# Kernel tuning notes

Hardware: AMD Instinct MI355X
Metric: run time of the kernel (lower is better)

The kernel has to match this reference:

```python
import jax, jax.numpy as jnp
import numpy as np

C = 128
NUM_GROUPS = 32
EPS = 1e-6


def setup_inputs() -> dict:
    key = jax.random.key(0)
    ks = jax.random.split(key, 6)
    B, H, W = 8, 64, 64
    x = jax.random.normal(ks[0], (B, C, H, W), dtype=jnp.float32)
    # 1x1 conv weights stored as [out_c, in_c] (kernel spatial dims are 1)
    fan_avg = C  # fan_in == fan_out == C for 1x1 conv
    bound = np.sqrt(3.0 / fan_avg)
    wq = jax.random.uniform(ks[1], (C, C), jnp.float32, -bound, bound)
    wk = jax.random.uniform(ks[2], (C, C), jnp.float32, -bound, bound)
    wv = jax.random.uniform(ks[3], (C, C), jnp.float32, -bound, bound)
    # proj_out has init_scale=0.0 -> near-zero init; use tiny random instead to test math
    wo = jax.random.uniform(ks[4], (C, C), jnp.float32, -bound, bound) * 1e-3
    bq = jnp.zeros((C,), jnp.float32)
    bk = jnp.zeros((C,), jnp.float32)
    bv = jnp.zeros((C,), jnp.float32)
    bo = jnp.zeros((C,), jnp.float32)
    gamma = jnp.ones((C,), jnp.float32)
    beta = jnp.zeros((C,), jnp.float32)
    return {"x": x, "gamma": gamma, "beta": beta,
            "wq": wq, "bq": bq, "wk": wk, "bk": bk,
            "wv": wv, "bv": bv, "wo": wo, "bo": bo}


def _group_norm(x, gamma, beta):
    B, Ch, H, W = x.shape
    g = NUM_GROUPS
    xg = x.reshape(B, g, Ch // g, H, W)
    mean = jnp.mean(xg, axis=(2, 3, 4), keepdims=True)
    var = jnp.var(xg, axis=(2, 3, 4), keepdims=True)
    xn = ((xg - mean) * jax.lax.rsqrt(var + EPS)).reshape(B, Ch, H, W)
    return xn * gamma[None, :, None, None] + beta[None, :, None, None]


def _conv1x1(x, w, b):
    # x: [B,C,H,W], w: [O,C], b: [O]
    return jnp.einsum('bchw,oc->bohw', x, w) + b[None, :, None, None]


def reference(x, gamma, beta, wq, bq, wk, bk, wv, bv, wo, bo):
    B, Ch, H, W = x.shape
    n = H * W
    h = _group_norm(x, gamma, beta)
    q = _conv1x1(h, wq, bq).reshape(B, Ch, n)
    k = _conv1x1(h, wk, bk).reshape(B, Ch, n)
    v = _conv1x1(h, wv, bv).reshape(B, Ch, n)
    # attn[b, i, j] = sum_c q[b,c,i] * k[b,c,j] / sqrt(C)
    attn = jnp.einsum('bci,bcj->bij', q, k) * (float(Ch) ** -0.5)
    attn = jax.nn.softmax(attn, axis=-1)
    # h[b,c,i] = sum_j v[b,c,j] * attn[b,i,j]
    out = jnp.einsum('bcj,bij->bci', v, attn).reshape(B, Ch, H, W)
    out = _conv1x1(out, wo, bo)
    return x + out
```

## Files before the change

kernel.cpp:

```cpp
#include <hip/hip_runtime.h>


typedef float f32x4 __attribute__((ext_vector_type(4)));
typedef short short8 __attribute__((ext_vector_type(8)));
typedef _Float16 half8 __attribute__((ext_vector_type(8)));
typedef _Float16 half2t __attribute__((ext_vector_type(2)));
typedef unsigned short ush;
typedef unsigned short ush4 __attribute__((ext_vector_type(4)));
typedef unsigned int uint4t __attribute__((ext_vector_type(4)));
typedef int int8v __attribute__((ext_vector_type(8)));

union V8U {
  uint4t h[2];
  int8v v;
};

__device__ __forceinline__ ush f2bf(float f) {
  unsigned u = __builtin_bit_cast(unsigned, f);
  u = (u + 0x7FFFu + ((u >> 16) & 1u)) >> 16;
  return (ush)u;
}
__device__ __forceinline__ float bf2f(ush v) {
  unsigned u = ((unsigned)v) << 16;
  return __builtin_bit_cast(float, u);
}
__device__ __forceinline__ unsigned f2fp8(float x) {
  unsigned u = __builtin_bit_cast(unsigned, x);
  unsigned s = (u >> 24) & 0x80u;
  unsigned au = u & 0x7fffffffu;
  if (au < 0x3A800000u) return s;
  if (au >= 0x43E00000u) return s | 0x7Eu;
  int e = (int)(au >> 23) - 127;
  if (e < -6) {
    float a = __builtin_bit_cast(float, au);
    int m = (int)(a * 512.0f + 0.5f);
    if (m >= 8) return s | 0x08u;
    return s | (unsigned)m;
  }
  unsigned keep = au >> 20, rem = au & 0xFFFFFu;
  keep += (rem > 0x80000u) || ((rem == 0x80000u) && (keep & 1u));
  int ef = (int)(keep >> 3) - 127;
  if (ef >= 8 && ((ef > 8) || ((keep & 7u) == 7u))) return s | 0x7Eu;
  return s | (unsigned)(((ef + 7) << 3) | (int)(keep & 7u));
}
__device__ __forceinline__ void async16(const void* g, void* l) {
  __builtin_amdgcn_global_load_lds(
      (const __attribute__((address_space(1))) unsigned int*)g,
      (__attribute__((address_space(3))) unsigned int*)l, 16, 0, 0);
}

__global__ __launch_bounds__(256) void gn_stats_kernel(
    const float* __restrict__ x, const float* __restrict__ gamma,
    const float* __restrict__ beta, const float* __restrict__ wo,
    const float* __restrict__ wq, const float* __restrict__ wk,
    const float* __restrict__ wv, float* __restrict__ scale_c,
    float* __restrict__ shift_c, ush* __restrict__ wobh,
    ush* __restrict__ wqb, ush* __restrict__ wkb, ush* __restrict__ wvb) {
  int bg = blockIdx.x;
  int b = bg >> 5, g = bg & 31;
  int tid = threadIdx.x;
  if (bg < 64) {
    int m = bg >> 4;
    int v4 = ((bg & 15) * 256 + tid) * 4;
    const float* src = m == 0 ? wo : (m == 1 ? wq : (m == 2 ? wk : wv));
    float4 w4 = *(const float4*)(src + v4);
    ush4 pk;
    if (m == 0) {
      pk.x = __builtin_bit_cast(ush, (_Float16)w4.x);
      pk.y = __builtin_bit_cast(ush, (_Float16)w4.y);
      pk.z = __builtin_bit_cast(ush, (_Float16)w4.z);
      pk.w = __builtin_bit_cast(ush, (_Float16)w4.w);
      *(ush4*)(wobh + v4) = pk;
    } else {
      pk.x = f2bf(w4.x); pk.y = f2bf(w4.y);
      pk.z = f2bf(w4.z); pk.w = f2bf(w4.w);
      ush* dst = m == 1 ? wqb : (m == 2 ? wkb : wvb);
      *(ush4*)(dst + v4) = pk;
    }
  }
  const float4* base = (const float4*)(x + (size_t)bg * 16384);
  float s = 0.f, sq = 0.f;
#pragma unroll
  for (int p = 0; p < 16; ++p) {
    float4 v = base[p * 256 + tid];
    s += (v.x + v.y) + (v.z + v.w);
    sq += (v.x * v.x + v.y * v.y) + (v.z * v.z + v.w * v.w);
  }
#pragma unroll
  for (int off = 32; off > 0; off >>= 1) {
    s += __shfl_down(s, off);
    sq += __shfl_down(sq, off);
  }
  __shared__ float rs[4], rq[4], mv[2];
  int w = tid >> 6, lane = tid & 63;
  if (lane == 0) { rs[w] = s; rq[w] = sq; }
  __syncthreads();
  if (tid == 0) {
    float S = (rs[0] + rs[1]) + (rs[2] + rs[3]);
    float Q = (rq[0] + rq[1]) + (rq[2] + rq[3]);
    float mean = S * (1.f / 16384.f);
    float var = Q * (1.f / 16384.f) - mean * mean;
    mv[0] = mean;
    mv[1] = rsqrtf(var + 1e-6f);
  }
  __syncthreads();
  if (tid < 4) {
    int c = (g << 2) + tid;
    float sc = mv[1] * gamma[c];
    scale_c[(b << 7) + c] = sc;
    shift_c[(b << 7) + c] = beta[c] - mv[0] * sc;
  }
}

__global__ __launch_bounds__(256) void qkv_kernel(
    const float* __restrict__ x, const float* __restrict__ scale_c,
    const float* __restrict__ shift_c, const ush* __restrict__ wqb,
    const ush* __restrict__ wkb, const ush* __restrict__ wvb,
    const float* __restrict__ bq, const float* __restrict__ bk,
    const float* __restrict__ bv, char* __restrict__ Qt8,
    char* __restrict__ Kt8, _Float16* __restrict__ Vh) {
  __shared__ __align__(16) ush hs[64 * 136];
  __shared__ __align__(16) ush wol[128 * 136];
  char* hs8 = (char*)hs;
  int bx = blockIdx.x;
  int type = bx >> 9;
  int rb = bx & 511;
  int b = rb >> 6, i0 = (rb & 63) << 6;
  int tid = threadIdx.x;
  int w = tid >> 6, lane = tid & 63, ln15 = lane & 15, quad = lane >> 4;

#pragma unroll
  for (int p = 0; p < 8; ++p) {
    int id = p * 256 + tid;
    int i = id & 63;
    int g8 = id >> 6;
    int c0 = g8 << 2;
    const float* xp = x + (((size_t)((b << 7) + c0)) << 12) + i0 + i;
    ush4 pk4;
#pragma unroll
    for (int e = 0; e < 4; ++e) {
      float h = xp[(size_t)e << 12] * scale_c[(b << 7) + c0 + e] +
                shift_c[(b << 7) + c0 + e];
      pk4[e] = f2bf(h);
    }
    int pg = g8 ^ ((i & 15) << 1);
    *(ush4*)(hs8 + i * 272 + pg * 8) = pk4;
  }
  const ush* Wb = type == 0 ? wqb : (type == 1 ? wkb : wvb);
#pragma unroll
  for (int p = 0; p < 8; ++p) {
    int cid = p * 256 + tid;
    int o = cid >> 4, ch = (cid & 15) << 3;
    *(uint4t*)&wol[o * 136 + ch] = *(const uint4t*)(Wb + (o << 7) + ch);
  }
  __syncthreads();

#define HS_FRAG(row, dc) \
  (*(const short8*)(hs8 + (row) * 272 + (((((dc)*4 + quad)) ^ ((row)&15)) << 4)))

  if (type < 2) {
    f32x4 acc[8] = {};
    int hrow = w * 16 + ln15;
#pragma unroll
    for (int dc = 0; dc < 4; ++dc) {
      short8 af = HS_FRAG(hrow, dc);
#pragma unroll
      for (int nb = 0; nb < 8; ++nb) {
        short8 bf = *(const short8*)&wol[(nb * 16 + ln15) * 136 + dc * 32 + quad * 8];
        acc[nb] = __builtin_amdgcn_mfma_f32_16x16x32_bf16(af, bf, acc[nb], 0, 0, 0);
      }
    }
    const float* bias = type == 0 ? bq : bk;
    char* dst8 = type == 0 ? Qt8 : Kt8;
    __syncthreads();
#pragma unroll
    for (int nb = 0; nb < 8; ++nb) {
      int o = nb * 16 + ln15;
      float bi = bias[o];
#pragma unroll
      for (int r = 0; r < 4; ++r) {
        float val = acc[nb][r] + bi;
        if (type == 0) val *= 0.12751742f;
        hs8[(w * 16 + quad * 4 + r) * 144 + o] = (char)f2fp8(val);
      }
    }
    __syncthreads();
    int i = tid >> 2, seg = tid & 3;
    uint4 d0 = *(const uint4*)(hs8 + i * 144 + seg * 32);
    uint4 d1 = *(const uint4*)(hs8 + i * 144 + seg * 32 + 16);
    char* drow = dst8 + (((size_t)((b << 12) + i0 + i)) << 7) + seg * 32;
    *(uint4*)drow = d0;
    *(uint4*)(drow + 16) = d1;
  } else {
    f32x4 acc[8] = {};
    int hrow = w * 16 + ln15;
#pragma unroll
    for (int dc = 0; dc < 4; ++dc) {
      short8 bf = HS_FRAG(hrow, dc);
#pragma unroll
      for (int mb = 0; mb < 8; ++mb) {
        short8 af = *(const short8*)&wol[(mb * 16 + ln15) * 136 + dc * 32 + quad * 8];
        acc[mb] = __builtin_amdgcn_mfma_f32_16x16x32_bf16(af, bf, acc[mb], 0, 0, 0);
      }
    }
#pragma unroll
    for (int mb = 0; mb < 8; ++mb) {
#pragma unroll
      for (int r = 0; r < 4; ++r) {
        int o = mb * 16 + quad * 4 + r;
        float val = acc[mb][r] + bv[o];
        Vh[(((size_t)((b << 7) + o)) << 12) + i0 + w * 16 + ln15] = (_Float16)val;
      }
    }
  }
#undef HS_FRAG
}

__global__ __launch_bounds__(256, 2) void attn_kernel(
    const char* __restrict__ Qt8, const char* __restrict__ Kt8,
    const _Float16* __restrict__ Vh, ush* __restrict__ po,
    float* __restrict__ lw) {
  __shared__ __align__(16) char ksb[2][4096];
  __shared__ __align__(16) _Float16 vsb[2][4096];
  int bx = blockIdx.x;
  int b = bx & 7, qt = (bx >> 3) & 15, ksid = bx >> 7;
  int tid = threadIdx.x;
  int w = tid >> 6, lane = tid & 63, ln15 = lane & 15, quad = lane >> 4;
  int qbase = (qt << 8) + (w << 6);
  int j0 = ksid << 10;

  int8v qf[4];
#pragma unroll
  for (int ih = 0; ih < 4; ++ih) {
    const char* qrow =
        Qt8 + (((size_t)((b << 12) + qbase + ih * 16 + ln15)) << 7) + quad * 32;
    V8U u;
    u.h[0] = *(const uint4t*)(qrow);
    u.h[1] = *(const uint4t*)(qrow + 16);
    qf[ih] = u.v;
  }

  int kj = (w << 3) + (lane >> 3);
  int kh = (kj & 3) | (((kj >> 3) & 1) << 2);
  int kg = (lane & 7) ^ kh;
  const char* ksrc = Kt8 + (((size_t)((b << 12) + j0 + kj)) << 7) + (kg << 4);
  int d0r = (w << 5) + (lane >> 2);
  int d1r = d0r + 16;
  int vg0 = (lane & 3) ^ (((d0r >> 1) + (d0r >> 3)) & 3);
  int vg1 = (lane & 3) ^ (((d1r >> 1) + (d1r >> 3)) & 3);
  const _Float16* vsrc0 =
      Vh + (((size_t)((b << 7) + d0r)) << 12) + j0 + (vg0 << 3);
  const _Float16* vsrc1 =
      Vh + (((size_t)((b << 7) + d1r)) << 12) + j0 + (vg1 << 3);
  char* kdA = &ksb[0][0] + (w << 10);
  char* kdB = &ksb[1][0] + (w << 10);
  char* vdA0 = (char*)&vsb[0][0] + ((w * 2 + 0) << 10);
  char* vdA1 = (char*)&vsb[0][0] + ((w * 2 + 1) << 10);
  char* vdB0 = (char*)&vsb[1][0] + ((w * 2 + 0) << 10);
  char* vdB1 = (char*)&vsb[1][0] + ((w * 2 + 1) << 10);

  async16(ksrc, kdA);
  async16(vsrc0, vdA0);
  async16(vsrc1, vdA1);
  __syncthreads();

  f32x4 O[4][8] = {};
  float lsum[4] = {0.f, 0.f, 0.f, 0.f};
  const f32x4 SINIT = {-7.2134752f, -7.2134752f, -7.2134752f, -7.2134752f};
  int r0 = ((ln15 >> 2) << 3) + (ln15 & 3), r1 = r0 + 4;
  int hr = (ln15 & 3) | (((ln15 >> 2) & 1) << 2);
  int g0 = ((2 * quad) ^ hr) << 4;
  int g1 = ((2 * quad + 1) ^ hr) << 4;

  for (int jt = 0; jt < 32; ++jt) {
    int buf = jt & 1;
    if (jt + 1 < 32) {
      ksrc += 4096;
      vsrc0 += 32;
      vsrc1 += 32;
      if (buf == 0) {
        async16(ksrc, kdB);
        async16(vsrc0, vdB0);
        async16(vsrc1, vdB1);
      } else {
        async16(ksrc, kdA);
        async16(vsrc0, vdA0);
        async16(vsrc1, vdA1);
      }
    }
    const char* kb = &ksb[buf][0];
    const char* vb = (const char*)&vsb[buf][0];

    V8U ka, kc;
    ka.h[0] = *(const uint4t*)(kb + r0 * 128 + g0);
    ka.h[1] = *(const uint4t*)(kb + r0 * 128 + g1);
    kc.h[0] = *(const uint4t*)(kb + r1 * 128 + g0);
    kc.h[1] = *(const uint4t*)(kb + r1 * 128 + g1);
    f32x4 S[4][2];
#pragma unroll
    for (int ih = 0; ih < 4; ++ih) {
      S[ih][0] = __builtin_amdgcn_mfma_scale_f32_16x16x128_f8f6f4(
          ka.v, qf[ih], SINIT, 0, 0, 0, 0x7F7F7F7F, 0, 0x7F7F7F7F);
      S[ih][1] = __builtin_amdgcn_mfma_scale_f32_16x16x128_f8f6f4(
          kc.v, qf[ih], SINIT, 0, 0, 0, 0x7F7F7F7F, 0, 0x7F7F7F7F);
    }

    half8 pf[4];
#pragma unroll
    for (int ih = 0; ih < 4; ++ih) {
      float p0 = __builtin_amdgcn_exp2f(S[ih][0][0]);
      float p1 = __builtin_amdgcn_exp2f(S[ih][0][1]);
      float p2 = __builtin_amdgcn_exp2f(S[ih][0][2]);
      float p3 = __builtin_amdgcn_exp2f(S[ih][0][3]);
      float p4 = __builtin_amdgcn_exp2f(S[ih][1][0]);
      float p5 = __builtin_amdgcn_exp2f(S[ih][1][1]);
      float p6 = __builtin_amdgcn_exp2f(S[ih][1][2]);
      float p7 = __builtin_amdgcn_exp2f(S[ih][1][3]);
      lsum[ih] += ((p0 + p1) + (p2 + p3)) + ((p4 + p5) + (p6 + p7));
      uint4t pw;
      pw.x = __builtin_bit_cast(unsigned, __builtin_amdgcn_cvt_pkrtz(p0, p1));
      pw.y = __builtin_bit_cast(unsigned, __builtin_amdgcn_cvt_pkrtz(p2, p3));
      pw.z = __builtin_bit_cast(unsigned, __builtin_amdgcn_cvt_pkrtz(p4, p5));
      pw.w = __builtin_bit_cast(unsigned, __builtin_amdgcn_cvt_pkrtz(p6, p7));
      pf[ih] = __builtin_bit_cast(half8, pw);
    }
#pragma unroll
    for (int nb = 0; nb < 8; ++nb) {
      int d = nb * 16 + ln15;
      int sd = ((d >> 1) + (d >> 3)) & 3;
      half8 vf = *(const half8*)(vb + d * 64 + ((quad ^ sd) << 4));
#pragma unroll
      for (int ih = 0; ih < 4; ++ih)
        O[ih][nb] = __builtin_amdgcn_mfma_f32_16x16x32_f16(vf, pf[ih], O[ih][nb], 0, 0, 0);
    }
    __syncthreads();
  }

#pragma unroll
  for (int ih = 0; ih < 4; ++ih) {
    float l = lsum[ih];
    l += __shfl_xor(l, 16);
    l += __shfl_xor(l, 32);
    if (quad == 0) lw[(ksid << 15) + (b << 12) + qbase + ih * 16 + ln15] = l;
    int i = qbase + ih * 16 + ln15;
    size_t rowb = (((size_t)((ksid * 8 + b)) << 12) + i) << 7;
#pragma unroll
    for (int nb = 0; nb < 8; ++nb) {
      ush4 pk;
      pk.x = __builtin_bit_cast(ush, (_Float16)O[ih][nb][0]);
      pk.y = __builtin_bit_cast(ush, (_Float16)O[ih][nb][1]);
      pk.z = __builtin_bit_cast(ush, (_Float16)O[ih][nb][2]);
      pk.w = __builtin_bit_cast(ush, (_Float16)O[ih][nb][3]);
      *(ush4*)(po + rowb + nb * 16 + quad * 4) = pk;
    }
  }
}

__global__ __launch_bounds__(256) void proj_kernel(
    const float* __restrict__ x, const ush* __restrict__ po,
    const float* __restrict__ lw, const ush* __restrict__ wobh,
    const float* __restrict__ bo, float* __restrict__ out) {
  int bx = blockIdx.x;
  int oh = bx & 1;
  int bi = bx >> 1;
  int b = bi >> 6, i0 = (bi & 63) << 6;
  int tid = threadIdx.x;
  int w = tid >> 6, lane = tid & 63, ln15 = lane & 15, quad = lane >> 4;
  int i = i0 + w * 16 + ln15;
  float rl = 0.f;
#pragma unroll
  for (int s = 0; s < 4; ++s) rl += lw[(s << 15) + (b << 12) + i];
  _Float16 rh = (_Float16)(1.f / rl);

  f32x4 acc[4] = {};
#pragma unroll
  for (int dc = 0; dc < 4; ++dc) {
    size_t base = ((size_t)i << 7) + dc * 32 + quad * 8;
    half8 vs = *(const half8*)(po + (((size_t)b) << 19) + base);
#pragma unroll
    for (int s = 1; s < 4; ++s)
      vs = vs + *(const half8*)(po + (((size_t)(s * 8 + b)) << 19) + base);
    half8 bfv = vs * rh;
#pragma unroll
    for (int mb = 0; mb < 4; ++mb) {
      half8 af = *(const half8*)&wobh[(((oh * 4 + mb) * 16 + ln15) << 7) +
                                      dc * 32 + quad * 8];
      acc[mb] = __builtin_amdgcn_mfma_f32_16x16x32_f16(af, bfv, acc[mb], 0, 0, 0);
    }
  }
#pragma unroll
  for (int mb = 0; mb < 4; ++mb) {
#pragma unroll
    for (int r = 0; r < 4; ++r) {
      int o = (oh * 4 + mb) * 16 + quad * 4 + r;
      size_t idx = (((size_t)(b << 7) + o) << 12) + i;
      out[idx] = x[idx] + acc[mb][r] + bo[o];
    }
  }
}

extern "C" void kernel_launch(void* const* d_in, const int* in_sizes, int n_in,
                              void* d_out, int out_size, void* d_ws,
                              size_t ws_size, hipStream_t stream) {
  const float* x = (const float*)d_in[0];
  const float* gamma = (const float*)d_in[1];
  const float* beta = (const float*)d_in[2];
  const float* wq = (const float*)d_in[3];
  const float* bq = (const float*)d_in[4];
  const float* wk = (const float*)d_in[5];
  const float* bk = (const float*)d_in[6];
  const float* wv = (const float*)d_in[7];
  const float* bv = (const float*)d_in[8];
  const float* wo = (const float*)d_in[9];
  const float* bo = (const float*)d_in[10];
  float* out = (float*)d_out;

  const size_t NE = (size_t)8 * 4096 * 128;
  char* Qt8 = (char*)d_ws;
  char* Kt8 = Qt8 + NE;
  _Float16* Vh = (_Float16*)(Kt8 + NE);
  ush* po = (ush*)(Vh + NE);
  float* lwp = (float*)(po + 4 * NE);
  float* scale_c = lwp + 4 * 32768;
  float* shift_c = scale_c + 1024;
  ush* wobh = (ush*)(shift_c + 1024);
  ush* wqb = wobh + 16384;
  ush* wkb = wqb + 16384;
  ush* wvb = wkb + 16384;

  gn_stats_kernel<<<256, 256, 0, stream>>>(x, gamma, beta, wo, wq, wk, wv,
                                           scale_c, shift_c, wobh, wqb, wkb,
                                           wvb);
  qkv_kernel<<<1536, 256, 0, stream>>>(x, scale_c, shift_c, wqb, wkb, wvb, bq,
                                       bk, bv, Qt8, Kt8, Vh);
  attn_kernel<<<512, 256, 0, stream>>>(Qt8, Kt8, Vh, po, lwp);
  proj_kernel<<<1024, 256, 0, stream>>>(x, po, lwp, wobh, bo, out);
}
```

Baseline: 186.4 us.

## Use FP8 for V and probabilities in attention PV matmul with larger key tiles

V is now stored as FP8 instead of FP16, and the softmax probabilities are packed to FP8. The P·V product uses the 16x16x128 scaled FP8 MFMA, which needs a per-wave LDS round-trip to reshape P into the operand layout. Key/value tiles grow from 32 to 128 keys per iteration, giving 8 iterations instead of 32 and fewer barriers. Costs are lower accuracy for P and V, and extra LDS traffic and footprint, about 72KB per block, which may limit occupancy.

```diff
diff --git a/kernel.cpp b/kernel.cpp
--- a/kernel.cpp
+++ b/kernel.cpp
@@ -4,7 +4,6 @@
 typedef float f32x4 __attribute__((ext_vector_type(4)));
 typedef short short8 __attribute__((ext_vector_type(8)));
 typedef _Float16 half8 __attribute__((ext_vector_type(8)));
-typedef _Float16 half2t __attribute__((ext_vector_type(2)));
 typedef unsigned short ush;
 typedef unsigned short ush4 __attribute__((ext_vector_type(4)));
 typedef unsigned int uint4t __attribute__((ext_vector_type(4)));
@@ -14,15 +13,15 @@
   uint4t h[2];
   int8v v;
 };
+union P8U {
+  unsigned long long l[4];
+  int8v v;
+};
 
 __device__ __forceinline__ ush f2bf(float f) {
   unsigned u = __builtin_bit_cast(unsigned, f);
   u = (u + 0x7FFFu + ((u >> 16) & 1u)) >> 16;
   return (ush)u;
-}
-__device__ __forceinline__ float bf2f(ush v) {
-  unsigned u = ((unsigned)v) << 16;
-  return __builtin_bit_cast(float, u);
 }
 __device__ __forceinline__ unsigned f2fp8(float x) {
   unsigned u = __builtin_bit_cast(unsigned, x);
@@ -118,7 +117,7 @@
     const ush* __restrict__ wkb, const ush* __restrict__ wvb,
     const float* __restrict__ bq, const float* __restrict__ bk,
     const float* __restrict__ bv, char* __restrict__ Qt8,
-    char* __restrict__ Kt8, _Float16* __restrict__ Vh) {
+    char* __restrict__ Kt8, char* __restrict__ Vh8) {
   __shared__ __align__(16) ush hs[64 * 136];
   __shared__ __align__(16) ush wol[128 * 136];
   char* hs8 = (char*)hs;
@@ -209,7 +208,8 @@
       for (int r = 0; r < 4; ++r) {
         int o = mb * 16 + quad * 4 + r;
         float val = acc[mb][r] + bv[o];
-        Vh[(((size_t)((b << 7) + o)) << 12) + i0 + w * 16 + ln15] = (_Float16)val;
+        Vh8[(((size_t)((b << 7) + o)) << 12) + i0 + w * 16 + ln15] =
+            (char)f2fp8(val);
       }
     }
   }
@@ -218,10 +218,9 @@
 
 __global__ __launch_bounds__(256, 2) void attn_kernel(
     const char* __restrict__ Qt8, const char* __restrict__ Kt8,
-    const _Float16* __restrict__ Vh, ush* __restrict__ po,
+    const char* __restrict__ Vh8, ush* __restrict__ po,
     float* __restrict__ lw) {
-  __shared__ __align__(16) char ksb[2][4096];
-  __shared__ __align__(16) _Float16 vsb[2][4096];
+  __shared__ __align__(16) char smem[73728];
   int bx = blockIdx.x;
   int b = bx & 7, qt = (bx >> 3) & 15, ksid = bx >> 7;
   int tid = threadIdx.x;
@@ -244,24 +243,23 @@
   int kh = (kj & 3) | (((kj >> 3) & 1) << 2);
   int kg = (lane & 7) ^ kh;
   const char* ksrc = Kt8 + (((size_t)((b << 12) + j0 + kj)) << 7) + (kg << 4);
-  int d0r = (w << 5) + (lane >> 2);
-  int d1r = d0r + 16;
-  int vg0 = (lane & 3) ^ (((d0r >> 1) + (d0r >> 3)) & 3);
-  int vg1 = (lane & 3) ^ (((d1r >> 1) + (d1r >> 3)) & 3);
-  const _Float16* vsrc0 =
-      Vh + (((size_t)((b << 7) + d0r)) << 12) + j0 + (vg0 << 3);
-  const _Float16* vsrc1 =
-      Vh + (((size_t)((b << 7) + d1r)) << 12) + j0 + (vg1 << 3);
-  char* kdA = &ksb[0][0] + (w << 10);
-  char* kdB = &ksb[1][0] + (w << 10);
-  char* vdA0 = (char*)&vsb[0][0] + ((w * 2 + 0) << 10);
-  char* vdA1 = (char*)&vsb[0][0] + ((w * 2 + 1) << 10);
-  char* vdB0 = (char*)&vsb[1][0] + ((w * 2 + 0) << 10);
-  char* vdB1 = (char*)&vsb[1][0] + ((w * 2 + 1) << 10);
-
-  async16(ksrc, kdA);
-  async16(vsrc0, vdA0);
-  async16(vsrc1, vdA1);
+  int vrow = (w << 3) + (lane >> 3);
+  int hv_dma = ((lane >> 3) & 3) | ((w & 1) << 2);
+  int vgd = (lane & 7) ^ hv_dma;
+  const char* vsrc =
+      Vh8 + (((size_t)((b << 7) + vrow)) << 12) + j0 + (vgd << 4);
+
+  char* Kb0 = smem;
+  char* Kb1 = smem + 16384;
+  char* Vb0 = smem + 32768;
+  char* Vb1 = smem + 49152;
+  char* Pw = smem + 65536 + (w << 11);
+
+#pragma unroll
+  for (int c = 0; c < 4; ++c) {
+    async16(ksrc + c * 4096, Kb0 + c * 4096 + (w << 10));
+    async16(vsrc + (size_t)c * 131072, Vb0 + c * 4096 + (w << 10));
+  }
   __syncthreads();
 
   f32x4 O[4][8] = {};
@@ -271,67 +269,84 @@
   int hr = (ln15 & 3) | (((ln15 >> 2) & 1) << 2);
   int g0 = ((2 * quad) ^ hr) << 4;
   int g1 = ((2 * quad + 1) ^ hr) << 4;
-
-  for (int jt = 0; jt < 32; ++jt) {
+  int hv_r = (ln15 & 3) | (((ln15 >> 3) & 1) << 2);
+  int vg0 = ((2 * quad) ^ hv_r) << 4;
+  int vg1 = ((2 * quad + 1) ^ hv_r) << 4;
+
+  unsigned pf8a[4][4][2];
+
+  for (int jt = 0; jt < 8; ++jt) {
     int buf = jt & 1;
-    if (jt + 1 < 32) {
-      ksrc += 4096;
-      vsrc0 += 32;
-      vsrc1 += 32;
-      if (buf == 0) {
-        async16(ksrc, kdB);
-        async16(vsrc0, vdB0);
-        async16(vsrc1, vdB1);
-      } else {
-        async16(ksrc, kdA);
-        async16(vsrc0, vdA0);
-        async16(vsrc1, vdA1);
-      }
-    }
-    const char* kb = &ksb[buf][0];
-    const char* vb = (const char*)&vsb[buf][0];
-
-    V8U ka, kc;
-    ka.h[0] = *(const uint4t*)(kb + r0 * 128 + g0);
-    ka.h[1] = *(const uint4t*)(kb + r0 * 128 + g1);
-    kc.h[0] = *(const uint4t*)(kb + r1 * 128 + g0);
-    kc.h[1] = *(const uint4t*)(kb + r1 * 128 + g1);
-    f32x4 S[4][2];
+    char* Kbc = buf ? Kb1 : Kb0;
+    char* Vbc = buf ? Vb1 : Vb0;
+    if (jt < 7) {
+      ksrc += 16384;
+      vsrc += 128;
+      char* Kbn = buf ? Kb0 : Kb1;
+      char* Vbn = buf ? Vb0 : Vb1;
+#pragma unroll
+      for (int c = 0; c < 4; ++c) {
+        async16(ksrc + c * 4096, Kbn + c * 4096 + (w << 10));
+        async16(vsrc + (size_t)c * 131072, Vbn + c * 4096 + (w << 10));
+      }
+    }
+
+#pragma unroll
+    for (int s = 0; s < 4; ++s) {
+      const char* kb = Kbc + s * 4096;
+      V8U ka, kc;
+      ka.h[0] = *(const uint4t*)(kb + r0 * 128 + g0);
+      ka.h[1] = *(const uint4t*)(kb + r0 * 128 + g1);
+      kc.h[0] = *(const uint4t*)(kb + r1 * 128 + g0);
+      kc.h[1] = *(const uint4t*)(kb + r1 * 128 + g1);
+#pragma unroll
+      for (int ih = 0; ih < 4; ++ih) {
+        f32x4 S0 = __builtin_amdgcn_mfma_scale_f32_16x16x128_f8f6f4(
+            ka.v, qf[ih], SINIT, 0, 0, 0, 0x7F7F7F7F, 0, 0x7F7F7F7F);
+        f32x4 S1 = __builtin_amdgcn_mfma_scale_f32_16x16x128_f8f6f4(
+            kc.v, qf[ih], SINIT, 0, 0, 0, 0x7F7F7F7F, 0, 0x7F7F7F7F);
+        float p0 = __builtin_amdgcn_exp2f(S0[0]);
+        float p1 = __builtin_amdgcn_exp2f(S0[1]);
+        float p2 = __builtin_amdgcn_exp2f(S0[2]);
+        float p3 = __builtin_amdgcn_exp2f(S0[3]);
+        float p4 = __builtin_amdgcn_exp2f(S1[0]);
+        float p5 = __builtin_amdgcn_exp2f(S1[1]);
+        float p6 = __builtin_amdgcn_exp2f(S1[2]);
+        float p7 = __builtin_amdgcn_exp2f(S1[3]);
+        lsum[ih] += ((p0 + p1) + (p2 + p3)) + ((p4 + p5) + (p6 + p7));
+        unsigned lo = (unsigned)__builtin_amdgcn_cvt_pk_fp8_f32(p0, p1, 0, false);
+        lo = (unsigned)__builtin_amdgcn_cvt_pk_fp8_f32(p2, p3, (int)lo, true);
+        unsigned hi = (unsigned)__builtin_amdgcn_cvt_pk_fp8_f32(p4, p5, 0, false);
+        hi = (unsigned)__builtin_amdgcn_cvt_pk_fp8_f32(p6, p7, (int)hi, true);
+        pf8a[ih][s][0] = lo;
+        pf8a[ih][s][1] = hi;
+      }
+    }
+
 #pragma unroll
     for (int ih = 0; ih < 4; ++ih) {
-      S[ih][0] = __builtin_amdgcn_mfma_scale_f32_16x16x128_f8f6f4(
-          ka.v, qf[ih], SINIT, 0, 0, 0, 0x7F7F7F7F, 0, 0x7F7F7F7F);
-      S[ih][1] = __builtin_amdgcn_mfma_scale_f32_16x16x128_f8f6f4(
-          kc.v, qf[ih], SINIT, 0, 0, 0, 0x7F7F7F7F, 0, 0x7F7F7F7F);
-    }
-
-    half8 pf[4];
-#pragma unroll
-    for (int ih = 0; ih < 4; ++ih) {
-      float p0 = __builtin_amdgcn_exp2f(S[ih][0][0]);
-      float p1 = __builtin_amdgcn_exp2f(S[ih][0][1]);
-      float p2 = __builtin_amdgcn_exp2f(S[ih][0][2]);
-      float p3 = __builtin_amdgcn_exp2f(S[ih][0][3]);
-      float p4 = __builtin_amdgcn_exp2f(S[ih][1][0]);
-      float p5 = __builtin_amdgcn_exp2f(S[ih][1][1]);
-      float p6 = __builtin_amdgcn_exp2f(S[ih][1][2]);
-      float p7 = __builtin_amdgcn_exp2f(S[ih][1][3]);
-      lsum[ih] += ((p0 + p1) + (p2 + p3)) + ((p4 + p5) + (p6 + p7));
-      uint4t pw;
-      pw.x = __builtin_bit_cast(unsigned, __builtin_amdgcn_cvt_pkrtz(p0, p1));
-      pw.y = __builtin_bit_cast(unsigned, __builtin_amdgcn_cvt_pkrtz(p2, p3));
-      pw.z = __builtin_bit_cast(unsigned, __builtin_amdgcn_cvt_pkrtz(p4, p5));
-      pw.w = __builtin_bit_cast(unsigned, __builtin_amdgcn_cvt_pkrtz(p6, p7));
-      pf[ih] = __builtin_bit_cast(half8, pw);
-    }
-#pragma unroll
-    for (int nb = 0; nb < 8; ++nb) {
-      int d = nb * 16 + ln15;
-      int sd = ((d >> 1) + (d >> 3)) & 3;
-      half8 vf = *(const half8*)(vb + d * 64 + ((quad ^ sd) << 4));
-#pragma unroll
-      for (int ih = 0; ih < 4; ++ih)
-        O[ih][nb] = __builtin_amdgcn_mfma_f32_16x16x32_f16(vf, pf[ih], O[ih][nb], 0, 0, 0);
+#pragma unroll
+      for (int s = 0; s < 4; ++s) {
+        unsigned long long pr =
+            ((unsigned long long)pf8a[ih][s][1] << 32) | pf8a[ih][s][0];
+        *(unsigned long long*)(Pw + ln15 * 128 +
+                               ((((s << 2) + quad) ^ ln15) << 3)) = pr;
+      }
+      P8U pu;
+#pragma unroll
+      for (int c = 0; c < 4; ++c)
+        pu.l[c] = *(const unsigned long long*)(
+            Pw + ln15 * 128 + ((((quad << 2) + c) ^ ln15) << 3));
+      int8v pfv = pu.v;
+#pragma unroll
+      for (int nb = 0; nb < 8; ++nb) {
+        int d = nb * 16 + ln15;
+        V8U va;
+        va.h[0] = *(const uint4t*)(Vbc + d * 128 + vg0);
+        va.h[1] = *(const uint4t*)(Vbc + d * 128 + vg1);
+        O[ih][nb] = __builtin_amdgcn_mfma_scale_f32_16x16x128_f8f6f4(
+            va.v, pfv, O[ih][nb], 0, 0, 0, 0x7F7F7F7F, 0, 0x7F7F7F7F);
+      }
     }
     __syncthreads();
   }
@@ -418,8 +433,8 @@
   const size_t NE = (size_t)8 * 4096 * 128;
   char* Qt8 = (char*)d_ws;
   char* Kt8 = Qt8 + NE;
-  _Float16* Vh = (_Float16*)(Kt8 + NE);
-  ush* po = (ush*)(Vh + NE);
+  char* Vh8 = Kt8 + NE;
+  ush* po = (ush*)(Vh8 + NE);
   float* lwp = (float*)(po + 4 * NE);
   float* scale_c = lwp + 4 * 32768;
   float* shift_c = scale_c + 1024;
@@ -432,7 +447,7 @@
                                            scale_c, shift_c, wobh, wqb, wkb,
                                            wvb);
   qkv_kernel<<<1536, 256, 0, stream>>>(x, scale_c, shift_c, wqb, wkb, wvb, bq,
-                                       bk, bv, Qt8, Kt8, Vh);
-  attn_kernel<<<512, 256, 0, stream>>>(Qt8, Kt8, Vh, po, lwp);
+                                       bk, bv, Qt8, Kt8, Vh8);
+  attn_kernel<<<512, 256, 0, stream>>>(Qt8, Kt8, Vh8, po, lwp);
   proj_kernel<<<1024, 256, 0, stream>>>(x, po, lwp, wobh, bo, out);
 }
```

New measurement: 252.1 us. 1.35x slower.
